# Optimization experiments

Measured on AMD Instinct MI355X. Metric: run time of the kernel, lower is better.

Reference implementation:

```python
import jax, jax.numpy as jnp
from jax import lax
import numpy as np

IN_CH, OUT_CH, K, STRIDE = 4, 256, 16, 8
D_STATE, D_CONV, EXPAND, HEADDIM = 128, 4, 2, 64
D_INNER = EXPAND * OUT_CH            # 512
NHEADS = D_INNER // HEADDIM          # 8
CONV_DIM = D_INNER + 2 * D_STATE     # 768 (ngroups=1)
D_IN_PROJ = 2 * D_INNER + 2 * D_STATE + NHEADS  # 1288
B_SZ, L = 8, 16384


def _conv1d(x, w, b, stride, padding):
    y = lax.conv_general_dilated(x, w, (stride,), padding,
                                 dimension_numbers=('NCH', 'OIH', 'NCH'))
    return y + b[None, :, None]


def _mamba2(u, in_proj_w, conv1d_w, conv1d_b, dt_bias, A_log, D_skip, norm_w, out_proj_w):
    # u: (b, l, d_model). Faithful Mamba2 forward (ngroups=1, rmsnorm gated, no biases on projections).
    b, l, _ = u.shape
    zxbcdt = jnp.einsum('bld,ed->ble', u, in_proj_w)           # (b, l, d_in_proj)
    z = zxbcdt[..., :D_INNER]
    xBC = zxbcdt[..., D_INNER:D_INNER + CONV_DIM]
    dt = jax.nn.softplus(zxbcdt[..., D_INNER + CONV_DIM:] + dt_bias)  # (b, l, h)
    # causal depthwise conv (torch pads d_conv-1 both sides then truncates to :l == left-pad only) + SiLU
    xBC = lax.conv_general_dilated(xBC.transpose(0, 2, 1), conv1d_w, (1,),
                                   [(D_CONV - 1, 0)], feature_group_count=CONV_DIM,
                                   dimension_numbers=('NCH', 'OIH', 'NCH'))
    xBC = jax.nn.silu((xBC + conv1d_b[None, :, None]).transpose(0, 2, 1))  # (b, l, conv_dim)
    xs = xBC[..., :D_INNER].reshape(b, l, NHEADS, HEADDIM)
    Bm = xBC[..., D_INNER:D_INNER + D_STATE]                   # (b, l, n)
    Cm = xBC[..., D_INNER + D_STATE:]                          # (b, l, n)
    A = -jnp.exp(A_log)                                        # (h,), scalar A per head
    dA = jnp.exp(dt * A)                                       # (b, l, h)

    def step(h, inp):
        dA_t, dt_t, x_t, B_t, C_t = inp
        h = h * dA_t[:, :, None, None] + jnp.einsum('bh,bhp,bn->bhpn', dt_t, x_t, B_t)
        return h, jnp.einsum('bhpn,bn->bhp', h, C_t)

    h0 = jnp.zeros((b, NHEADS, HEADDIM, D_STATE), dtype=u.dtype)
    _, ys = lax.scan(step, h0, (dA.swapaxes(0, 1), dt.swapaxes(0, 1),
                                xs.swapaxes(0, 1), Bm.swapaxes(0, 1), Cm.swapaxes(0, 1)))
    y = ys.swapaxes(0, 1) + D_skip[None, None, :, None] * xs   # (b, l, h, p)
    y = y.reshape(b, l, D_INNER) * jax.nn.silu(z)              # gated RMSNorm (norm_before_gate=False)
    y = y * lax.rsqrt(jnp.mean(y * y, axis=-1, keepdims=True) + 1e-5) * norm_w
    return jnp.einsum('ble,de->bld', y, out_proj_w)


def _forward(x, conv_w, conv_b, in_proj_w, conv1d_w, conv1d_b, dt_bias, A_log,
             D_skip, norm_w, out_proj_w, conv1_w, conv1_b, convT_w, convT_b):
    h = jax.nn.relu(_conv1d(x, conv_w, conv_b, STRIDE, 'VALID'))       # (b, out_ch, l')
    y = _mamba2(h.transpose(0, 2, 1), in_proj_w, conv1d_w, conv1d_b,
                dt_bias, A_log, D_skip, norm_w, out_proj_w)
    y = y.transpose(0, 2, 1)                                           # (b, out_ch, l')
    y = _conv1d(y, conv1_w, conv1_b, 1, [(7, 8)])  # torch padding='same', even kernel: left=7, right=8
    # ConvTranspose1d: torch weight (Cin, Cout, K) -> flipped OIH kernel + lhs dilation
    kern = jnp.flip(convT_w, -1).transpose(1, 0, 2)
    y = lax.conv_general_dilated(y, kern, (1,), [(K - 1, K - 1)], lhs_dilation=(STRIDE,),
                                 dimension_numbers=('NCH', 'OIH', 'NCH'))
    return y + convT_b[None, :, None]


def setup_inputs() -> dict:
    key = jax.random.key(0)
    ks = jax.random.split(key, 16)
    n = lambda k, shp, sc=0.05: jax.random.normal(k, shp, dtype=jnp.float32) * sc
    return {
        'x': jax.random.normal(ks[0], (B_SZ, IN_CH, L), dtype=jnp.float32),
        'conv_w': n(ks[1], (OUT_CH, IN_CH, K)),
        'conv_b': n(ks[2], (OUT_CH,)),
        'in_proj_w': n(ks[3], (D_IN_PROJ, OUT_CH)),
        'conv1d_w': n(ks[4], (CONV_DIM, 1, D_CONV), 0.3),
        'conv1d_b': n(ks[5], (CONV_DIM,), 0.1),
        'dt_bias': n(ks[6], (NHEADS,), 0.5),
        'A_log': jnp.log(jax.random.uniform(ks[7], (NHEADS,), minval=1.0, maxval=16.0)),
        'D_skip': n(ks[8], (NHEADS,), 1.0),
        'norm_w': jnp.ones((D_INNER,), dtype=jnp.float32),
        'out_proj_w': n(ks[9], (OUT_CH, D_INNER)),
        'conv1_w': n(ks[10], (STRIDE, OUT_CH, K)),
        'conv1_b': n(ks[11], (STRIDE,)),
        'convT_w': n(ks[12], (STRIDE, IN_CH, K)),
        'convT_b': n(ks[13], (IN_CH,)),
    }


def reference(x, conv_w, conv_b, in_proj_w, conv1d_w, conv1d_b, dt_bias, A_log,
              D_skip, norm_w, out_proj_w, conv1_w, conv1_b, convT_w, convT_b):
    return _forward(x, conv_w, conv_b, in_proj_w, conv1d_w, conv1d_b, dt_bias, A_log,
                    D_skip, norm_w, out_proj_w, conv1_w, conv1_b, convT_w, convT_b)
```

## Files before the change

kernel.cpp:

```cpp
#include <hip/hip_runtime.h>
#include <cstddef>
#include <cstdint>

constexpr int L_IN   = 16384;
constexpr int L_SEQ  = 2047;
constexpr int BATCH  = 8;
constexpr int M_TOK  = BATCH * L_SEQ;
constexpr int D_INNER = 512;
constexpr int NHEADS  = 8;
constexpr int HEADDIM = 64;
constexpr int D_STATE = 128;
constexpr int CONV_DIM = 768;
constexpr int D_IN_PROJ = 1288;

constexpr int QC  = 64;
constexpr int NCH = 32;

constexpr size_t OFF_U    = 0;
constexpr size_t OFF_PB   = OFF_U   + 2096128;
constexpr size_t OFF_ZB   = OFF_U   + 4192256;
constexpr size_t OFF_XBC  = OFF_ZB  + 4192256;
constexpr size_t OFF_DT   = OFF_XBC + 6288384;
constexpr size_t OFF_AW   = OFF_DT  + 131008;
constexpr size_t OFF_XC   = OFF_AW  + 131008;
constexpr size_t OFF_Y    = OFF_XC  + 6288384;
constexpr size_t OFF_YC1  = OFF_Y   + 4192256;
constexpr size_t OFF_PBUF = OFF_YC1 + 131008;
constexpr size_t OFF_HS   = OFF_PBUF + 2048;
constexpr size_t OFF_WBIN = OFF_HS  + 8388608;
constexpr size_t OFF_WBF  = OFF_WBIN + 164864;
constexpr size_t OFF_W2   = OFF_WBF + 8192;

using short8 = __attribute__((ext_vector_type(8))) short;
using f32x4  = __attribute__((ext_vector_type(4))) float;
typedef unsigned short ushort_t;

__device__ __forceinline__ ushort_t f2bf(float f) {
  uint32_t u = __float_as_uint(f);
  u += 0x7fffu + ((u >> 16) & 1u);
  return (ushort_t)(u >> 16);
}
__device__ __forceinline__ float bf2f(ushort_t h) {
  return __uint_as_float(((uint32_t)h) << 16);
}
#define MFMA16(a, b, c) __builtin_amdgcn_mfma_f32_16x16x32_bf16(a, b, c, 0, 0, 0)

__global__ __launch_bounds__(256) void k_prep(const float* __restrict__ x,
    const float* __restrict__ w1, const float* __restrict__ w3,
    const float* __restrict__ conv1_w, const float* __restrict__ wout,
    ushort_t* __restrict__ PB, ushort_t* __restrict__ o1, ushort_t* __restrict__ o3,
    ushort_t* __restrict__ W2b) {
  const int bid = blockIdx.x;
  const int tid = threadIdx.x;
  if (bid < 512) {
    int idx = bid * 256 + tid;
    if (idx >= M_TOK * 8) return;
    int oct = idx & 7, row = idx >> 3;
    int t = row % L_SEQ, b = row / L_SEQ;
    int ic = oct >> 1, k0 = (oct & 1) * 8;
    const float* src = x + ((size_t)b * 4 + ic) * L_IN + t * 8 + k0;
    float4 a0 = *(const float4*)src;
    float4 a1 = *(const float4*)(src + 4);
    short8 o;
    o[0] = (short)f2bf(a0.x); o[1] = (short)f2bf(a0.y);
    o[2] = (short)f2bf(a0.z); o[3] = (short)f2bf(a0.w);
    o[4] = (short)f2bf(a1.x); o[5] = (short)f2bf(a1.y);
    o[6] = (short)f2bf(a1.z); o[7] = (short)f2bf(a1.w);
    *(short8*)(PB + (size_t)row * 64 + oct * 8) = o;
  } else if (bid < 1800) {
    int i = (bid - 512) * 256 + tid;
    if (i < D_IN_PROJ * 256) o1[i] = f2bf(w1[i]);
    if (i < 256 * 64)        o3[i] = f2bf(w3[i]);
  } else {
    const int r = bid - 1800;
    const int oc = r >> 4, k = r & 15;
    const int d0 = tid;
    float acc0 = 0.f, acc1 = 0.f;
    for (int o = 0; o < 256; o++) {
      float wv = conv1_w[((size_t)oc * 256 + o) * 16 + k];
      acc0 = fmaf(wv, wout[(size_t)o * 512 + d0], acc0);
      acc1 = fmaf(wv, wout[(size_t)o * 512 + d0 + 256], acc1);
    }
    W2b[(size_t)r * 512 + d0]       = f2bf(acc0);
    W2b[(size_t)r * 512 + d0 + 256] = f2bf(acc1);
  }
}

template<int EPI>
__global__ __launch_bounds__(256) void gemm_bf16(const ushort_t* __restrict__ A, int lda,
    const ushort_t* __restrict__ B, int ldb, float* __restrict__ C,
    const float* __restrict__ bias, int M, int N, int K,
    ushort_t* __restrict__ zb, ushort_t* __restrict__ xbcb,
    float* __restrict__ dtb, float* __restrict__ awb,
    const float* __restrict__ dt_bias, const float* __restrict__ A_log) {
  __shared__ __attribute__((aligned(16))) ushort_t sA[128 * 64];
  __shared__ __attribute__((aligned(16))) ushort_t sB[128 * 64];
  const int tid = threadIdx.x;
  const int m0 = blockIdx.y * 128, n0 = blockIdx.x * 128;
  const int w = tid >> 6, lane = tid & 63;
  const int l15 = lane & 15, lK = lane >> 4;
  const int wr = w >> 1, wc = w & 1;
  f32x4 acc[4][4] = {};
  for (int k0 = 0; k0 < K; k0 += 64) {
    __syncthreads();
#pragma unroll
    for (int j = 0; j < 4; j++) {
      int idx = j * 256 + tid;
      int r = idx >> 3, s = idx & 7;
      short8 va = {0, 0, 0, 0, 0, 0, 0, 0};
      int gm = m0 + r;
      if (gm < M) va = *(const short8*)(A + (size_t)gm * lda + k0 + s * 8);
      *(short8*)&sA[r * 64 + ((s ^ (r & 7)) * 8)] = va;
      short8 vb = {0, 0, 0, 0, 0, 0, 0, 0};
      int gn = n0 + r;
      if (gn < N) vb = *(const short8*)(B + (size_t)gn * ldb + k0 + s * 8);
      *(short8*)&sB[r * 64 + ((s ^ (r & 7)) * 8)] = vb;
    }
    __syncthreads();
#pragma unroll
    for (int kk = 0; kk < 2; kk++) {
      short8 af[4], bf[4];
#pragma unroll
      for (int mt = 0; mt < 4; mt++) {
        int r = wr * 64 + mt * 16 + l15;
        af[mt] = *(const short8*)&sA[r * 64 + (((kk * 4 + lK) ^ (r & 7)) * 8)];
      }
#pragma unroll
      for (int nt = 0; nt < 4; nt++) {
        int r = wc * 64 + nt * 16 + l15;
        bf[nt] = *(const short8*)&sB[r * 64 + (((kk * 4 + lK) ^ (r & 7)) * 8)];
      }
#pragma unroll
      for (int mt = 0; mt < 4; mt++)
#pragma unroll
        for (int nt = 0; nt < 4; nt++)
          acc[mt][nt] = MFMA16(af[mt], bf[nt], acc[mt][nt]);
    }
  }
  if constexpr (EPI == 0) {
#pragma unroll
    for (int mt = 0; mt < 4; mt++)
#pragma unroll
      for (int i = 0; i < 4; i++) {
        int gm = m0 + wr * 64 + mt * 16 + lK * 4 + i;
        if (gm < M) {
          float* crow = C + (size_t)gm * N;
#pragma unroll
          for (int nt = 0; nt < 4; nt++) {
            int gn = n0 + wc * 64 + nt * 16 + l15;
            if (gn < N) crow[gn] = acc[mt][nt][i];
          }
        }
      }
  } else if constexpr (EPI == 1) {
    ushort_t* Cb = (ushort_t*)C;
#pragma unroll
    for (int mt = 0; mt < 4; mt++)
#pragma unroll
      for (int i = 0; i < 4; i++) {
        int gm = m0 + wr * 64 + mt * 16 + lK * 4 + i;
#pragma unroll
        for (int nt = 0; nt < 4; nt++) {
          int gn = n0 + wc * 64 + nt * 16 + l15;
          float v = fmaxf(acc[mt][nt][i] + bias[gn], 0.f);
          uint32_t mine = f2bf(v);
          uint32_t other = (uint32_t)__shfl_xor((int)mine, 1, 64);
          if (((lane & 1) == 0) && gm < M)
            *(uint32_t*)(Cb + (size_t)gm * N + gn) = mine | (other << 16);
        }
      }
  } else {
    if (n0 < 1280) {
      ushort_t* dst = (n0 < 512) ? zb : xbcb;
      const int ldd  = (n0 < 512) ? 512 : 768;
      const int coff = (n0 < 512) ? 0 : 512;
#pragma unroll
      for (int mt = 0; mt < 4; mt++)
#pragma unroll
        for (int i = 0; i < 4; i++) {
          int gm = m0 + wr * 64 + mt * 16 + lK * 4 + i;
#pragma unroll
          for (int nt = 0; nt < 4; nt++) {
            int gn = n0 + wc * 64 + nt * 16 + l15;
            uint32_t mine = f2bf(acc[mt][nt][i]);
            uint32_t other = (uint32_t)__shfl_xor((int)mine, 1, 64);
            if (((lane & 1) == 0) && gm < M)
              *(uint32_t*)(dst + (size_t)gm * ldd + (gn - coff)) = mine | (other << 16);
          }
        }
    } else {
#pragma unroll
      for (int mt = 0; mt < 4; mt++)
#pragma unroll
        for (int i = 0; i < 4; i++) {
          int gm = m0 + wr * 64 + mt * 16 + lK * 4 + i;
          if (gm >= M) continue;
#pragma unroll
          for (int nt = 0; nt < 4; nt++) {
            int gn = n0 + wc * 64 + nt * 16 + l15;
            if (gn < N) {
              int hd = gn - 1280;
              float v = acc[mt][nt][i] + dt_bias[hd];
              float sp = (v > 20.f) ? v : log1pf(expf(v));
              dtb[(size_t)gm * 8 + hd] = sp;
              awb[(size_t)gm * 8 + hd] = -expf(A_log[hd]) * sp;
            }
          }
        }
    }
  }
}

__global__ __launch_bounds__(192) void k_dw(const ushort_t* __restrict__ xbcb,
    const float* __restrict__ w, const float* __restrict__ bias,
    ushort_t* __restrict__ xcb) {
  const int bid = blockIdx.x;
  const int tb = bid & 511, b = bid >> 9;
  const int t0 = tb * 4;
  const int c = threadIdx.x * 4;
  const size_t rowb = (size_t)b * L_SEQ;
  float wr[4][4];
#pragma unroll
  for (int j = 0; j < 4; j++)
#pragma unroll
    for (int k = 0; k < 4; k++) wr[j][k] = w[(c + j) * 4 + k];
  const float4 bs = {bias[c], bias[c + 1], bias[c + 2], bias[c + 3]};
  float v[7][4];
#pragma unroll
  for (int r = 0; r < 7; r++) {
    int tt = t0 - 3 + r;
    if (tt >= 0 && tt < L_SEQ) {
      uint2 pk = *(const uint2*)(xbcb + (rowb + tt) * CONV_DIM + c);
      v[r][0] = bf2f((ushort_t)(pk.x & 0xffff));
      v[r][1] = bf2f((ushort_t)(pk.x >> 16));
      v[r][2] = bf2f((ushort_t)(pk.y & 0xffff));
      v[r][3] = bf2f((ushort_t)(pk.y >> 16));
    } else {
      v[r][0] = v[r][1] = v[r][2] = v[r][3] = 0.f;
    }
  }
#pragma unroll
  for (int o = 0; o < 4; o++) {
    int t = t0 + o;
    if (t >= L_SEQ) break;
    float a0 = bs.x, a1 = bs.y, a2 = bs.z, a3 = bs.w;
#pragma unroll
    for (int k = 0; k < 4; k++) {
      a0 = fmaf(v[o + k][0], wr[0][k], a0);
      a1 = fmaf(v[o + k][1], wr[1][k], a1);
      a2 = fmaf(v[o + k][2], wr[2][k], a2);
      a3 = fmaf(v[o + k][3], wr[3][k], a3);
    }
    float s0 = a0 / (1.f + expf(-a0));
    float s1 = a1 / (1.f + expf(-a1));
    float s2 = a2 / (1.f + expf(-a2));
    float s3 = a3 / (1.f + expf(-a3));
    uint2 ov;
    ov.x = (uint32_t)f2bf(s0) | ((uint32_t)f2bf(s1) << 16);
    ov.y = (uint32_t)f2bf(s2) | ((uint32_t)f2bf(s3) << 16);
    *(uint2*)(xcb + (rowb + t) * CONV_DIM + c) = ov;
  }
}

__global__ __launch_bounds__(256) void k_ssd_state(const ushort_t* __restrict__ xcb,
    const float* __restrict__ dtb, const float* __restrict__ aw,
    ushort_t* __restrict__ HSb, float* __restrict__ Pbuf) {
  const int ch = blockIdx.x, bh = blockIdx.y;
  const int b = bh >> 3, h = bh & 7;
  const int t0 = ch * QC;
  const int valid = (L_SEQ - t0 < QC) ? (L_SEQ - t0) : QC;
  const size_t rowbase = (size_t)b * L_SEQ;
  __shared__ __attribute__((aligned(16))) short sBT[128][72];
  __shared__ __attribute__((aligned(16))) short sXw[64][72];
  __shared__ float sW[64];
  __shared__ float sLtot;
  const int tid = threadIdx.x;
  if (tid < 64) {
    float aa = 0.f, dd = 0.f;
    if (tid < valid) { size_t r8 = (rowbase + t0 + tid) * 8 + h; aa = aw[r8]; dd = dtb[r8]; }
    float s = aa;
#pragma unroll
    for (int d = 1; d < 64; d <<= 1) { float o = __shfl_up(s, d, 64); if (tid >= d) s += o; }
    float Lt = __shfl(s, 63, 64);
    sW[tid] = expf(Lt - s) * dd;
    if (tid == 63) sLtot = s;
  }
  __syncthreads();
  for (int i = tid; i < 64 * 16; i += 256) {
    int r = i >> 4, q = (i & 15) * 8;
    short8 v = {0, 0, 0, 0, 0, 0, 0, 0};
    if (r < valid) v = *(const short8*)(xcb + (rowbase + t0 + r) * CONV_DIM + 512 + q);
#pragma unroll
    for (int j = 0; j < 8; j++) sBT[q + j][r] = v[j];
  }
  for (int i = tid; i < 64 * 8; i += 256) {
    int r = i >> 3, q = (i & 7) * 8;
    short8 v = {0, 0, 0, 0, 0, 0, 0, 0};
    if (r < valid) v = *(const short8*)(xcb + (rowbase + t0 + r) * CONV_DIM + h * 64 + q);
    float wv = sW[r];
#pragma unroll
    for (int j = 0; j < 8; j++) sXw[q + j][r] = (short)f2bf(bf2f((ushort_t)v[j]) * wv);
  }
  __syncthreads();
  const int w = tid >> 6, l15 = tid & 15, lK = (tid & 63) >> 4;
  f32x4 acc[2][4] = {};
  short8 afr[2][2];
#pragma unroll
  for (int j = 0; j < 2; j++)
#pragma unroll
    for (int kt = 0; kt < 2; kt++)
      afr[j][kt] = *(const short8*)&sBT[(w * 2 + j) * 16 + l15][kt * 32 + lK * 8];
#pragma unroll
  for (int pt = 0; pt < 4; pt++) {
#pragma unroll
    for (int kt = 0; kt < 2; kt++) {
      short8 bfr = *(const short8*)&sXw[pt * 16 + l15][kt * 32 + lK * 8];
      acc[0][pt] = MFMA16(afr[0][kt], bfr, acc[0][pt]);
      acc[1][pt] = MFMA16(afr[1][kt], bfr, acc[1][pt]);
    }
  }
  ushort_t* dst = HSb + ((size_t)bh * NCH + ch) * 8192;
#pragma unroll
  for (int j = 0; j < 2; j++)
#pragma unroll
    for (int pt = 0; pt < 4; pt++)
#pragma unroll
      for (int i = 0; i < 4; i++) {
        int n = (w * 2 + j) * 16 + lK * 4 + i, p = pt * 16 + l15;
        uint32_t mine = f2bf(acc[j][pt][i]);
        uint32_t other = (uint32_t)__shfl_xor((int)mine, 1, 64);
        if ((l15 & 1) == 0)
          *(uint32_t*)(dst + n * 64 + p) = mine | (other << 16);
      }
  if (tid == 0) Pbuf[bh * NCH + ch] = expf(sLtot);
}

__global__ __launch_bounds__(256) void k_ssd_comb(ushort_t* __restrict__ HSb,
                                                  const float* __restrict__ Pbuf) {
  const int bh = blockIdx.y;
  const int e2 = blockIdx.x * 256 + threadIdx.x;
  float run0 = 0.f, run1 = 0.f;
  for (int c = 0; c < NCH; c++) {
    size_t idx = ((size_t)bh * NCH + c) * 8192 + (size_t)e2 * 2;
    uint32_t pk = *(const uint32_t*)(HSb + idx);
    float P = Pbuf[bh * NCH + c];
    run0 = fmaf(P, run0, bf2f((ushort_t)(pk & 0xffff)));
    run1 = fmaf(P, run1, bf2f((ushort_t)(pk >> 16)));
    *(uint32_t*)(HSb + idx) = (uint32_t)f2bf(run0) | ((uint32_t)f2bf(run1) << 16);
  }
}

__global__ __launch_bounds__(256) void k_ssd_y(const ushort_t* __restrict__ xcb,
    const float* __restrict__ dtb, const float* __restrict__ aw,
    const float* __restrict__ Dskip, const ushort_t* __restrict__ HSb,
    ushort_t* __restrict__ y16) {
  const int ch = blockIdx.x, bh = blockIdx.y;
  const int b = bh >> 3, h = bh & 7;
  const int t0 = ch * QC;
  const int valid = (L_SEQ - t0 < QC) ? (L_SEQ - t0) : QC;
  const size_t rowbase = (size_t)b * L_SEQ;
  __shared__ __attribute__((aligned(16))) short sB[64][136];
  __shared__ __attribute__((aligned(16))) short sC[64][136];
  __shared__ __attribute__((aligned(16))) short sH[64][136];
  __shared__ __attribute__((aligned(16))) short sX[64][72];
  __shared__ float sLrel[64], sdt[64], sEL[64];
  short (*sM)[72] = (short(*)[72])&sB[0][0];
  const int tid = threadIdx.x;
  if (tid < 64) {
    float aa = 0.f, dd = 0.f;
    if (tid < valid) { size_t r8 = (rowbase + t0 + tid) * 8 + h; aa = aw[r8]; dd = dtb[r8]; }
    float s = aa;
#pragma unroll
    for (int d = 1; d < 64; d <<= 1) { float o = __shfl_up(s, d, 64); if (tid >= d) s += o; }
    sLrel[tid] = s; sdt[tid] = dd; sEL[tid] = expf(s);
  }
  for (int i = tid; i < 64 * 16; i += 256) {
    int r = i >> 4, q = (i & 15) * 8;
    short8 vb = {0, 0, 0, 0, 0, 0, 0, 0}, vc = {0, 0, 0, 0, 0, 0, 0, 0};
    if (r < valid) {
      const ushort_t* rp = xcb + (rowbase + t0 + r) * CONV_DIM;
      vb = *(const short8*)(rp + 512 + q);
      vc = *(const short8*)(rp + 640 + q);
    }
#pragma unroll
    for (int j = 0; j < 8; j++) { sB[r][q + j] = vb[j]; sC[r][q + j] = vc[j]; }
  }
  for (int i = tid; i < 64 * 8; i += 256) {
    int r = i >> 3, q = (i & 7) * 8;
    short8 v = {0, 0, 0, 0, 0, 0, 0, 0};
    if (r < valid) v = *(const short8*)(xcb + (rowbase + t0 + r) * CONV_DIM + h * 64 + q);
#pragma unroll
    for (int j = 0; j < 8; j++) sX[q + j][r] = v[j];
  }
  for (int i = tid; i < 128 * 8; i += 256) {
    int n = i >> 3, q = (i & 7) * 8;
    short8 v = {0, 0, 0, 0, 0, 0, 0, 0};
    if (ch > 0) v = *(const short8*)(HSb + ((size_t)bh * NCH + (ch - 1)) * 8192 + n * 64 + q);
#pragma unroll
    for (int j = 0; j < 8; j++) sH[q + j][n] = v[j];
  }
  __syncthreads();
  const int w = tid >> 6, l15 = tid & 15, lK = (tid & 63) >> 4;
  short8 aC[4];
#pragma unroll
  for (int kt = 0; kt < 4; kt++)
    aC[kt] = *(const short8*)&sC[w * 16 + l15][kt * 32 + lK * 8];
  f32x4 g[4] = {};
#pragma unroll
  for (int st = 0; st < 4; st++)
#pragma unroll
    for (int kt = 0; kt < 4; kt++)
      g[st] = MFMA16(aC[kt], *(const short8*)&sB[st * 16 + l15][kt * 32 + lK * 8], g[st]);
  __syncthreads();
#pragma unroll
  for (int st = 0; st < 4; st++)
#pragma unroll
    for (int i = 0; i < 4; i++) {
      int tt = w * 16 + lK * 4 + i, ss = st * 16 + l15;
      float f = (ss <= tt) ? expf(sLrel[tt] - sLrel[ss]) * sdt[ss] : 0.f;
      sM[tt][ss] = (short)f2bf(g[st][i] * f);
    }
  __syncthreads();
  f32x4 acc[4] = {};
#pragma unroll
  for (int pt = 0; pt < 4; pt++)
#pragma unroll
    for (int kt = 0; kt < 4; kt++)
      acc[pt] = MFMA16(aC[kt], *(const short8*)&sH[pt * 16 + l15][kt * 32 + lK * 8], acc[pt]);
#pragma unroll
  for (int pt = 0; pt < 4; pt++)
#pragma unroll
    for (int i = 0; i < 4; i++)
      acc[pt][i] *= sEL[w * 16 + lK * 4 + i];
  short8 aM[2];
#pragma unroll
  for (int kt = 0; kt < 2; kt++)
    aM[kt] = *(const short8*)&sM[w * 16 + l15][kt * 32 + lK * 8];
#pragma unroll
  for (int pt = 0; pt < 4; pt++)
#pragma unroll
    for (int kt = 0; kt < 2; kt++)
      acc[pt] = MFMA16(aM[kt], *(const short8*)&sX[pt * 16 + l15][kt * 32 + lK * 8], acc[pt]);
  const float Dsk = Dskip[h];
#pragma unroll
  for (int pt = 0; pt < 4; pt++)
#pragma unroll
    for (int i = 0; i < 4; i++) {
      int tt = w * 16 + lK * 4 + i;
      int pp = pt * 16 + l15;
      float v = acc[pt][i] + Dsk * bf2f((ushort_t)sX[pp][tt]);
      uint32_t mine = f2bf(v);
      uint32_t other = (uint32_t)__shfl_xor((int)mine, 1, 64);
      if (((l15 & 1) == 0) && tt < valid)
        *(uint32_t*)(y16 + (rowbase + t0 + tt) * D_INNER + h * 64 + pp) = mine | (other << 16);
    }
}

__global__ __launch_bounds__(256) void k_norm(ushort_t* __restrict__ y16,
    const ushort_t* __restrict__ zb, const float* __restrict__ norm_w) {
  const int row = blockIdx.x * 4 + (threadIdx.x >> 6);
  const int lane = threadIdx.x & 63;
  const int c0 = lane * 8;
  ushort_t* yrow = y16 + (size_t)row * D_INNER;
  short8 yv = *(const short8*)(yrow + c0);
  short8 zv = *(const short8*)(zb + (size_t)row * 512 + c0);
  float v[8];
  float ss = 0.f;
#pragma unroll
  for (int j = 0; j < 8; j++) {
    float z = bf2f((ushort_t)zv[j]);
    float g = z / (1.f + expf(-z));
    v[j] = bf2f((ushort_t)yv[j]) * g;
    ss += v[j] * v[j];
  }
#pragma unroll
  for (int m = 32; m >= 1; m >>= 1) ss += __shfl_xor(ss, m, 64);
  float scale = rsqrtf(ss * (1.f / 512.f) + 1e-5f);
  float4 nw0 = *(const float4*)(norm_w + c0);
  float4 nw1 = *(const float4*)(norm_w + c0 + 4);
  short8 o;
  o[0] = (short)f2bf(v[0] * scale * nw0.x); o[1] = (short)f2bf(v[1] * scale * nw0.y);
  o[2] = (short)f2bf(v[2] * scale * nw0.z); o[3] = (short)f2bf(v[3] * scale * nw0.w);
  o[4] = (short)f2bf(v[4] * scale * nw1.x); o[5] = (short)f2bf(v[5] * scale * nw1.y);
  o[6] = (short)f2bf(v[6] * scale * nw1.z); o[7] = (short)f2bf(v[7] * scale * nw1.w);
  *(short8*)(yrow + c0) = o;
}

__global__ void k_red(const float* __restrict__ Y, const float* __restrict__ b1,
                      float* __restrict__ yc1) {
  int idx = blockIdx.x * 256 + threadIdx.x;
  if (idx >= BATCH * 8 * L_SEQ) return;
  int t = idx % L_SEQ;
  int bj = idx / L_SEQ;
  int j = bj & 7, b = bj >> 3;
  float acc = b1[j];
  const float* Yb = Y + (size_t)b * L_SEQ * 128;
#pragma unroll
  for (int k = 0; k < 16; k++) {
    int tt = t - 7 + k;
    if (tt >= 0 && tt < L_SEQ) acc += Yb[(size_t)tt * 128 + j * 16 + k];
  }
  yc1[idx] = acc;
}

__global__ void k_convT(const float* __restrict__ yc1,
                        const float* __restrict__ wT,
                        const float* __restrict__ bT, float* __restrict__ out) {
  const int s = blockIdx.x * 256 + threadIdx.x;
  const int c = blockIdx.y, b = blockIdx.z;
  float acc = bT[c];
  const int k0 = (15 - (s & 7)) & 7;
#pragma unroll
  for (int dk = 0; dk < 2; dk++) {
    int k = k0 + 8 * dk;
    int num = s - 15 + k;
    int m = num >> 3;
    if (num >= 0 && m < L_SEQ) {
#pragma unroll
      for (int j = 0; j < 8; j++) {
        float v = yc1[((size_t)b * 8 + j) * L_SEQ + m];
        acc = fmaf(v, wT[((size_t)j * 4 + c) * 16 + (15 - k)], acc);
      }
    }
  }
  out[((size_t)b * 4 + c) * L_IN + s] = acc;
}

extern "C" void kernel_launch(void* const* d_in, const int* in_sizes, int n_in,
                              void* d_out, int out_size, void* d_ws, size_t ws_size,
                              hipStream_t stream) {
  const float* x         = (const float*)d_in[0];
  const float* conv_w    = (const float*)d_in[1];
  const float* conv_b    = (const float*)d_in[2];
  const float* in_proj_w = (const float*)d_in[3];
  const float* conv1d_w  = (const float*)d_in[4];
  const float* conv1d_b  = (const float*)d_in[5];
  const float* dt_bias   = (const float*)d_in[6];
  const float* A_log     = (const float*)d_in[7];
  const float* D_skip    = (const float*)d_in[8];
  const float* norm_w    = (const float*)d_in[9];
  const float* out_proj_w= (const float*)d_in[10];
  const float* conv1_w   = (const float*)d_in[11];
  const float* conv1_b   = (const float*)d_in[12];
  const float* convT_w   = (const float*)d_in[13];
  const float* convT_b   = (const float*)d_in[14];
  float* out = (float*)d_out;
  float* ws  = (float*)d_ws;

  ushort_t* ub   = (ushort_t*)(ws + OFF_U);
  ushort_t* PB   = (ushort_t*)(ws + OFF_PB);
  ushort_t* zb   = (ushort_t*)(ws + OFF_ZB);
  ushort_t* xbcb = (ushort_t*)(ws + OFF_XBC);
  float* dtb  = ws + OFF_DT;
  float* awb  = ws + OFF_AW;
  ushort_t* xcb = (ushort_t*)(ws + OFF_XC);
  ushort_t* y16 = (ushort_t*)(ws + OFF_Y);
  float* yc1  = ws + OFF_YC1;
  float* Pbuf = ws + OFF_PBUF;
  ushort_t* HSb = (ushort_t*)(ws + OFF_HS);
  ushort_t* wbin  = (ushort_t*)(ws + OFF_WBIN);
  ushort_t* wbf   = (ushort_t*)(ws + OFF_WBF);
  ushort_t* W2b   = (ushort_t*)(ws + OFF_W2);
  float* Yg   = ws + OFF_U;

  k_prep<<<dim3(1928), 256, 0, stream>>>(x, in_proj_w, conv_w, conv1_w, out_proj_w,
                                         PB, wbin, wbf, W2b);
  gemm_bf16<1><<<dim3(2, 128), 256, 0, stream>>>(PB, 64, wbf, 64, (float*)ub,
      conv_b, M_TOK, 256, 64, nullptr, nullptr, nullptr, nullptr, nullptr, nullptr);
  gemm_bf16<2><<<dim3(11, 128), 256, 0, stream>>>(ub, 256, wbin, 256, nullptr,
      nullptr, M_TOK, D_IN_PROJ, 256, zb, xbcb, dtb, awb, dt_bias, A_log);
  k_dw<<<dim3(BATCH * 512), 192, 0, stream>>>(xbcb, conv1d_w, conv1d_b, xcb);
  k_ssd_state<<<dim3(NCH, 64), 256, 0, stream>>>(xcb, dtb, awb, HSb, Pbuf);
  k_ssd_comb<<<dim3(16, 64), 256, 0, stream>>>(HSb, Pbuf);
  k_ssd_y<<<dim3(NCH, 64), 256, 0, stream>>>(xcb, dtb, awb, D_skip, HSb, y16);
  k_norm<<<dim3(M_TOK / 4), 256, 0, stream>>>(y16, zb, norm_w);
  gemm_bf16<0><<<dim3(1, 128), 256, 0, stream>>>(y16, 512, W2b, 512, Yg,
      nullptr, M_TOK, 128, D_INNER, nullptr, nullptr, nullptr, nullptr, nullptr, nullptr);
  k_red<<<dim3((BATCH * 8 * L_SEQ + 255) / 256), 256, 0, stream>>>(Yg, conv1_b, yc1);
  k_convT<<<dim3(64, 4, 8), 256, 0, stream>>>(yc1, convT_w, convT_b, out);
}
```

Before: 219.6 us.

## Use direct global-to-LDS loads, XCD-aware block swizzle, and batched loads in state combine

The bf16 GEMM tile loads now use global_load_lds to write straight into the XOR-swizzled shared layout, skipping the trip through registers, and the M/N bounds checks are removed. Blocks are launched on a 1D grid and remapped so that neighbouring tiles land on the same XCD, which should improve L2 reuse. The chunk-state combine kernel issues all 32 chunk loads up front, runs the scan in registers, then writes everything back, so load latency overlaps. Dropping the bounds checks means edge tiles read past the real rows into neighbouring workspace memory; this relies on the epilogue discarding those rows.

Result: faster. 199.2 us (-9.3%).

```diff
diff --git a/kernel.cpp b/kernel.cpp
--- a/kernel.cpp
+++ b/kernel.cpp
@@ -44,6 +44,10 @@
   return __uint_as_float(((uint32_t)h) << 16);
 }
 #define MFMA16(a, b, c) __builtin_amdgcn_mfma_f32_16x16x32_bf16(a, b, c, 0, 0, 0)
+
+#define GLD_LDS(gp, lp) __builtin_amdgcn_global_load_lds( \
+    (const __attribute__((address_space(1))) void*)(gp),  \
+    (__attribute__((address_space(3))) void*)(lp), 16, 0, 0)
 
 __global__ __launch_bounds__(256) void k_prep(const float* __restrict__ x,
     const float* __restrict__ w1, const float* __restrict__ w3,
@@ -89,14 +93,16 @@
 template<int EPI>
 __global__ __launch_bounds__(256) void gemm_bf16(const ushort_t* __restrict__ A, int lda,
     const ushort_t* __restrict__ B, int ldb, float* __restrict__ C,
-    const float* __restrict__ bias, int M, int N, int K,
+    const float* __restrict__ bias, int M, int N, int K, int nx,
     ushort_t* __restrict__ zb, ushort_t* __restrict__ xbcb,
     float* __restrict__ dtb, float* __restrict__ awb,
     const float* __restrict__ dt_bias, const float* __restrict__ A_log) {
   __shared__ __attribute__((aligned(16))) ushort_t sA[128 * 64];
   __shared__ __attribute__((aligned(16))) ushort_t sB[128 * 64];
   const int tid = threadIdx.x;
-  const int m0 = blockIdx.y * 128, n0 = blockIdx.x * 128;
+  const int cpx = gridDim.x >> 3;
+  const int swz = (blockIdx.x & 7) * cpx + (blockIdx.x >> 3);
+  const int m0 = (swz / nx) * 128, n0 = (swz % nx) * 128;
   const int w = tid >> 6, lane = tid & 63;
   const int l15 = lane & 15, lK = lane >> 4;
   const int wr = w >> 1, wc = w & 1;
@@ -106,15 +112,10 @@
 #pragma unroll
     for (int j = 0; j < 4; j++) {
       int idx = j * 256 + tid;
-      int r = idx >> 3, s = idx & 7;
-      short8 va = {0, 0, 0, 0, 0, 0, 0, 0};
-      int gm = m0 + r;
-      if (gm < M) va = *(const short8*)(A + (size_t)gm * lda + k0 + s * 8);
-      *(short8*)&sA[r * 64 + ((s ^ (r & 7)) * 8)] = va;
-      short8 vb = {0, 0, 0, 0, 0, 0, 0, 0};
-      int gn = n0 + r;
-      if (gn < N) vb = *(const short8*)(B + (size_t)gn * ldb + k0 + s * 8);
-      *(short8*)&sB[r * 64 + ((s ^ (r & 7)) * 8)] = vb;
+      int r = idx >> 3;
+      int ss = (idx & 7) ^ (r & 7);
+      GLD_LDS(A + (size_t)(m0 + r) * lda + k0 + ss * 8, &sA[(j * 256 + w * 64) * 8]);
+      GLD_LDS(B + (size_t)(n0 + r) * ldb + k0 + ss * 8, &sB[(j * 256 + w * 64) * 8]);
     }
     __syncthreads();
 #pragma unroll
@@ -339,15 +340,22 @@
                                                   const float* __restrict__ Pbuf) {
   const int bh = blockIdx.y;
   const int e2 = blockIdx.x * 256 + threadIdx.x;
+  const size_t base = (size_t)bh * NCH * 8192 + (size_t)e2 * 2;
+  uint32_t pk[NCH];
+  float P[NCH];
+#pragma unroll
+  for (int c = 0; c < NCH; c++) pk[c] = *(const uint32_t*)(HSb + base + (size_t)c * 8192);
+#pragma unroll
+  for (int c = 0; c < NCH; c++) P[c] = Pbuf[bh * NCH + c];
   float run0 = 0.f, run1 = 0.f;
+#pragma unroll
   for (int c = 0; c < NCH; c++) {
-    size_t idx = ((size_t)bh * NCH + c) * 8192 + (size_t)e2 * 2;
-    uint32_t pk = *(const uint32_t*)(HSb + idx);
-    float P = Pbuf[bh * NCH + c];
-    run0 = fmaf(P, run0, bf2f((ushort_t)(pk & 0xffff)));
-    run1 = fmaf(P, run1, bf2f((ushort_t)(pk >> 16)));
-    *(uint32_t*)(HSb + idx) = (uint32_t)f2bf(run0) | ((uint32_t)f2bf(run1) << 16);
-  }
+    run0 = fmaf(P[c], run0, bf2f((ushort_t)(pk[c] & 0xffff)));
+    run1 = fmaf(P[c], run1, bf2f((ushort_t)(pk[c] >> 16)));
+    pk[c] = (uint32_t)f2bf(run0) | ((uint32_t)f2bf(run1) << 16);
+  }
+#pragma unroll
+  for (int c = 0; c < NCH; c++) *(uint32_t*)(HSb + base + (size_t)c * 8192) = pk[c];
 }
 
 __global__ __launch_bounds__(256) void k_ssd_y(const ushort_t* __restrict__ xcb,
@@ -565,17 +573,17 @@
 
   k_prep<<<dim3(1928), 256, 0, stream>>>(x, in_proj_w, conv_w, conv1_w, out_proj_w,
                                          PB, wbin, wbf, W2b);
-  gemm_bf16<1><<<dim3(2, 128), 256, 0, stream>>>(PB, 64, wbf, 64, (float*)ub,
-      conv_b, M_TOK, 256, 64, nullptr, nullptr, nullptr, nullptr, nullptr, nullptr);
-  gemm_bf16<2><<<dim3(11, 128), 256, 0, stream>>>(ub, 256, wbin, 256, nullptr,
-      nullptr, M_TOK, D_IN_PROJ, 256, zb, xbcb, dtb, awb, dt_bias, A_log);
+  gemm_bf16<1><<<dim3(256), 256, 0, stream>>>(PB, 64, wbf, 64, (float*)ub,
+      conv_b, M_TOK, 256, 64, 2, nullptr, nullptr, nullptr, nullptr, nullptr, nullptr);
+  gemm_bf16<2><<<dim3(1408), 256, 0, stream>>>(ub, 256, wbin, 256, nullptr,
+      nullptr, M_TOK, D_IN_PROJ, 256, 11, zb, xbcb, dtb, awb, dt_bias, A_log);
   k_dw<<<dim3(BATCH * 512), 192, 0, stream>>>(xbcb, conv1d_w, conv1d_b, xcb);
   k_ssd_state<<<dim3(NCH, 64), 256, 0, stream>>>(xcb, dtb, awb, HSb, Pbuf);
   k_ssd_comb<<<dim3(16, 64), 256, 0, stream>>>(HSb, Pbuf);
   k_ssd_y<<<dim3(NCH, 64), 256, 0, stream>>>(xcb, dtb, awb, D_skip, HSb, y16);
   k_norm<<<dim3(M_TOK / 4), 256, 0, stream>>>(y16, zb, norm_w);
-  gemm_bf16<0><<<dim3(1, 128), 256, 0, stream>>>(y16, 512, W2b, 512, Yg,
-      nullptr, M_TOK, 128, D_INNER, nullptr, nullptr, nullptr, nullptr, nullptr, nullptr);
+  gemm_bf16<0><<<dim3(128), 256, 0, stream>>>(y16, 512, W2b, 512, Yg,
+      nullptr, M_TOK, 128, D_INNER, 1, nullptr, nullptr, nullptr, nullptr, nullptr, nullptr);
   k_red<<<dim3((BATCH * 8 * L_SEQ + 255) / 256), 256, 0, stream>>>(Yg, conv1_b, yc1);
   k_convT<<<dim3(64, 4, 8), 256, 0, stream>>>(yc1, convT_w, convT_b, out);
 }
```
